# Performance work log

Hardware: AMD Instinct MI355X
Metric: run time of the kernel (lower is better)

## Reference

```python
import jax, jax.numpy as jnp
import numpy as np

B, L, N = 128, 4096, 256
MZ_MIN, MZ_MAX = 100.0, 1000.0
STD_DEV = 0.5 * (MZ_MAX - MZ_MIN) / N  # default std_dev from __init__
THRESH_LOW_WEIGHT = -10.0


def setup_inputs() -> dict:
    key = jax.random.key(0)
    k1, k2, k3 = jax.random.split(key, 3)
    # PeakSense.__init__: means = linspace(mz_min, mz_max, n_vals) + Normal(0, 0.5*std_dev)
    mu = jnp.linspace(MZ_MIN, MZ_MAX, N, dtype=jnp.float32) \
         + (0.5 * STD_DEV) * jax.random.normal(k1, (N,), dtype=jnp.float32)
    # log_vars filled with 2*log(std_dev)
    lv = jnp.full((N,), 2.0 * float(np.log(STD_DEV)), dtype=jnp.float32)
    # spectra: masses in [mz_min, mz_max] (sorted, as real centroided spectra are), positive intensities
    masses = MZ_MIN + (MZ_MAX - MZ_MIN) * jax.random.uniform(k2, (B, L), dtype=jnp.float32)
    masses = jnp.sort(masses, axis=1)
    intensities = jax.random.uniform(k3, (B, L), dtype=jnp.float32)
    return {"mu": mu, "lv": lv, "masses": masses, "intensities": intensities}


def reference(mu, lv, masses, intensities):
    # out[b, p] = sum_i exp(-0.5*(mz[b,i]-mu[p])^2 * exp(-lv[p])) * iv[b,i],
    # where terms with arg < THRESH_LOW_WEIGHT are dropped (kernel early-exit).
    inv_s2 = jnp.exp(-lv)                                  # [N], 1/sigma^2
    d = masses[:, :, None] - mu[None, None, :]             # [B, L, N]
    arg = (-0.5) * (d * d) * inv_s2                        # [B, L, N]
    w = jnp.where(arg >= THRESH_LOW_WEIGHT, jnp.exp(arg), jnp.zeros((), arg.dtype))
    return jnp.einsum('bln,bl->bn', w, intensities)        # [B, N]
```

## Files before the change

kernel.cpp:

```cpp
#include <hip/hip_runtime.h>
#include <math.h>


#define BLOCK 256
#define SUB 2
#define PPB (BLOCK / SUB)
#define MAXL 4096
#define THRESH -10.0f

__global__ __launch_bounds__(BLOCK) void peaksense_kernel(
    const float* __restrict__ mu,
    const float* __restrict__ lv,
    const float* __restrict__ masses,
    const float* __restrict__ inten,
    float* __restrict__ out,
    int B, int L, int N)
{
    __shared__ float2 s[MAXL];

    const int pg = blockIdx.x;
    const int b  = blockIdx.y;
    const int t  = threadIdx.x;

    const float* __restrict__ mrow = masses + (size_t)b * L;
    const float* __restrict__ irow = inten  + (size_t)b * L;
    for (int i = t; i < L; i += BLOCK)
        s[i] = make_float2(mrow[i], irow[i]);
    __syncthreads();

    const int lp  = t >> 1;
    const int sub = t & 1;
    const int p   = pg * PPB + lp;
    if (p >= N) return;

    const float mu_p = mu[p];
    const float lvp  = lv[p];
    const float inv  = __expf(-lvp);
    const float nh   = -0.5f * inv;
    const float r    = sqrtf(20.0f / inv) * 1.00001f + 1e-3f;
    const float tlo  = mu_p - r;
    const float thi  = mu_p + r;

    int lo = 0, hi = L;
    while (lo < hi) {
        int mid = (lo + hi) >> 1;
        if (s[mid].x < tlo) lo = mid + 1; else hi = mid;
    }
    const int start = lo;
    int lo2 = start, hi2 = L;
    while (lo2 < hi2) {
        int mid = (lo2 + hi2) >> 1;
        if (s[mid].x <= thi) lo2 = mid + 1; else hi2 = mid;
    }
    const int end = lo2;

    float acc = 0.0f;
    for (int i = start + sub; i < end; i += SUB) {
        const float2 v = s[i];
        const float d   = v.x - mu_p;
        const float arg = d * d * nh;
        if (arg >= THRESH)
            acc += __expf(arg) * v.y;
    }
    acc += __shfl_xor(acc, 1);
    if (sub == 0)
        out[(size_t)b * N + p] = acc;
}

extern "C" void kernel_launch(void* const* d_in, const int* in_sizes, int n_in,
                              void* d_out, int out_size, void* d_ws, size_t ws_size,
                              hipStream_t stream) {
    const float* mu     = (const float*)d_in[0];
    const float* lv     = (const float*)d_in[1];
    const float* masses = (const float*)d_in[2];
    const float* inten  = (const float*)d_in[3];
    float* out = (float*)d_out;

    const int N = in_sizes[0];
    const int B = out_size / N;
    const int L = in_sizes[2] / B;

    const int pgroups = (N + PPB - 1) / PPB;
    dim3 grid(pgroups, B);
    peaksense_kernel<<<grid, BLOCK, 0, stream>>>(mu, lv, masses, inten, out, B, L, N);
}
```

Baseline: 70.01 us.

## Overlap binary search with vectorized row loads and split bounds search across lanes

```diff
diff --git a/kernel.cpp b/kernel.cpp
--- a/kernel.cpp
+++ b/kernel.cpp
@@ -3,7 +3,7 @@
 
 
 #define BLOCK 256
-#define SUB 2
+#define SUB 4
 #define PPB (BLOCK / SUB)
 #define MAXL 4096
 #define THRESH -10.0f
@@ -24,46 +24,73 @@
 
     const float* __restrict__ mrow = masses + (size_t)b * L;
     const float* __restrict__ irow = inten  + (size_t)b * L;
-    for (int i = t; i < L; i += BLOCK)
-        s[i] = make_float2(mrow[i], irow[i]);
-    __syncthreads();
 
-    const int lp  = t >> 1;
-    const int sub = t & 1;
-    const int p   = pg * PPB + lp;
-    if (p >= N) return;
+    const bool fast = (L == MAXL);
 
-    const float mu_p = mu[p];
-    const float lvp  = lv[p];
+    float4 m0, m1, m2, m3, i0, i1, i2, i3;
+    if (fast) {
+        const float4* __restrict__ mrow4 = reinterpret_cast<const float4*>(mrow);
+        const float4* __restrict__ irow4 = reinterpret_cast<const float4*>(irow);
+        m0 = mrow4[t];             i0 = irow4[t];
+        m1 = mrow4[t +   BLOCK];   i1 = irow4[t +   BLOCK];
+        m2 = mrow4[t + 2*BLOCK];   i2 = irow4[t + 2*BLOCK];
+        m3 = mrow4[t + 3*BLOCK];   i3 = irow4[t + 3*BLOCK];
+    } else {
+        for (int i = t; i < L; i += BLOCK)
+            s[i] = make_float2(mrow[i], irow[i]);
+    }
+
+    const int  lp     = t >> 2;
+    const int  sub    = t & 3;
+    const int  p      = pg * PPB + lp;
+    const bool active = (p < N);
+    const int  pc     = active ? p : (N - 1);
+
+    const float mu_p = mu[pc];
+    const float lvp  = lv[pc];
     const float inv  = __expf(-lvp);
     const float nh   = -0.5f * inv;
     const float r    = sqrtf(20.0f / inv) * 1.00001f + 1e-3f;
     const float tlo  = mu_p - r;
     const float thi  = mu_p + r;
 
+    const bool  isHi   = sub & 1;
+    const float target = isHi ? thi : tlo;
     int lo = 0, hi = L;
     while (lo < hi) {
-        int mid = (lo + hi) >> 1;
-        if (s[mid].x < tlo) lo = mid + 1; else hi = mid;
+        const int   mid = (lo + hi) >> 1;
+        const float v   = mrow[mid];
+        const bool  go  = isHi ? (v <= target) : (v < target);
+        if (go) lo = mid + 1; else hi = mid;
     }
-    const int start = lo;
-    int lo2 = start, hi2 = L;
-    while (lo2 < hi2) {
-        int mid = (lo2 + hi2) >> 1;
-        if (s[mid].x <= thi) lo2 = mid + 1; else hi2 = mid;
+    const int other = __shfl_xor(lo, 1);
+    const int start = isHi ? other : lo;
+    const int end   = isHi ? lo    : other;
+
+    if (fast) {
+        float4* __restrict__ s4 = reinterpret_cast<float4*>(s);
+        s4[2*t]                   = make_float4(m0.x, i0.x, m0.y, i0.y);
+        s4[2*t + 1]               = make_float4(m0.z, i0.z, m0.w, i0.w);
+        s4[2*(t +   BLOCK)]       = make_float4(m1.x, i1.x, m1.y, i1.y);
+        s4[2*(t +   BLOCK) + 1]   = make_float4(m1.z, i1.z, m1.w, i1.w);
+        s4[2*(t + 2*BLOCK)]       = make_float4(m2.x, i2.x, m2.y, i2.y);
+        s4[2*(t + 2*BLOCK) + 1]   = make_float4(m2.z, i2.z, m2.w, i2.w);
+        s4[2*(t + 3*BLOCK)]       = make_float4(m3.x, i3.x, m3.y, i3.y);
+        s4[2*(t + 3*BLOCK) + 1]   = make_float4(m3.z, i3.z, m3.w, i3.w);
     }
-    const int end = lo2;
+    __syncthreads();
 
     float acc = 0.0f;
     for (int i = start + sub; i < end; i += SUB) {
-        const float2 v = s[i];
+        const float2 v  = s[i];
         const float d   = v.x - mu_p;
         const float arg = d * d * nh;
         if (arg >= THRESH)
             acc += __expf(arg) * v.y;
     }
     acc += __shfl_xor(acc, 1);
-    if (sub == 0)
+    acc += __shfl_xor(acc, 2);
+    if (sub == 0 && active)
         out[(size_t)b * N + p] = acc;
 }
 
```

New measurement: 68.89 us. No clear change (-1.6%).

## Drop shared-memory staging; branchless binary search and 8-way split per peak

Applied to the files above, without the earlier changes.

```diff
diff --git a/kernel.cpp b/kernel.cpp
--- a/kernel.cpp
+++ b/kernel.cpp
@@ -3,9 +3,8 @@
 
 
 #define BLOCK 256
-#define SUB 2
+#define SUB 8
 #define PPB (BLOCK / SUB)
-#define MAXL 4096
 #define THRESH -10.0f
 
 __global__ __launch_bounds__(BLOCK) void peaksense_kernel(
@@ -16,54 +15,54 @@
     float* __restrict__ out,
     int B, int L, int N)
 {
-    __shared__ float2 s[MAXL];
-
     const int pg = blockIdx.x;
     const int b  = blockIdx.y;
     const int t  = threadIdx.x;
 
     const float* __restrict__ mrow = masses + (size_t)b * L;
     const float* __restrict__ irow = inten  + (size_t)b * L;
-    for (int i = t; i < L; i += BLOCK)
-        s[i] = make_float2(mrow[i], irow[i]);
-    __syncthreads();
 
-    const int lp  = t >> 1;
-    const int sub = t & 1;
-    const int p   = pg * PPB + lp;
-    if (p >= N) return;
+    const int  lp     = t >> 3;
+    const int  sub    = t & 7;
+    const int  p      = pg * PPB + lp;
+    const bool active = (p < N);
+    const int  pc     = active ? p : (N - 1);
 
-    const float mu_p = mu[p];
-    const float lvp  = lv[p];
+    const float mu_p = mu[pc];
+    const float lvp  = lv[pc];
     const float inv  = __expf(-lvp);
     const float nh   = -0.5f * inv;
     const float r    = sqrtf(20.0f / inv) * 1.00001f + 1e-3f;
     const float tlo  = mu_p - r;
     const float thi  = mu_p + r;
 
-    int lo = 0, hi = L;
-    while (lo < hi) {
-        int mid = (lo + hi) >> 1;
-        if (s[mid].x < tlo) lo = mid + 1; else hi = mid;
+    int c0 = 0, c1 = 0;
+    const int step0 = L > 0 ? (1 << (31 - __clz(L))) : 0;
+    #pragma unroll
+    for (int step = step0; step > 0; step >>= 1) {
+        const int i0 = c0 + step;
+        const int i1 = c1 + step;
+        const bool ok0 = (i0 <= L) && (mrow[i0 - 1] <  tlo);
+        const bool ok1 = (i1 <= L) && (mrow[i1 - 1] <= thi);
+        if (ok0) c0 = i0;
+        if (ok1) c1 = i1;
     }
-    const int start = lo;
-    int lo2 = start, hi2 = L;
-    while (lo2 < hi2) {
-        int mid = (lo2 + hi2) >> 1;
-        if (s[mid].x <= thi) lo2 = mid + 1; else hi2 = mid;
-    }
-    const int end = lo2;
+    const int start = c0;
+    const int end   = c1;
 
     float acc = 0.0f;
     for (int i = start + sub; i < end; i += SUB) {
-        const float2 v = s[i];
-        const float d   = v.x - mu_p;
+        const float m   = mrow[i];
+        const float w   = irow[i];
+        const float d   = m - mu_p;
         const float arg = d * d * nh;
         if (arg >= THRESH)
-            acc += __expf(arg) * v.y;
+            acc += __expf(arg) * w;
     }
     acc += __shfl_xor(acc, 1);
-    if (sub == 0)
+    acc += __shfl_xor(acc, 2);
+    acc += __shfl_xor(acc, 4);
+    if (sub == 0 && active)
         out[(size_t)b * N + p] = acc;
 }
 
```

Result: slower. 73.47 us (+4.9%).
